# Performance work log

Hardware: AMD Instinct MI355X
Metric: run time of the kernel (lower is better)

Reference implementation:

```python
import jax, jax.numpy as jnp
import numpy as np
from jax import lax

B, N, C = 8, 16384, 4
NUM_GROUPS = 128
GROUP_SIZE = 32
GROUP_RADIUS = 0.1
UPSCALE_K = 128
OVERLAP_FACTOR = 0.7


def setup_inputs() -> dict:
    key = jax.random.key(0)
    k1, k2 = jax.random.split(key)
    # xyz in [0,1]^3, energy in [0,1] at channel 3
    points = jax.random.uniform(k1, (B, N, C), dtype=jnp.float32)
    lengths = jax.random.randint(k2, (B,), N // 2, N + 1).astype(jnp.int32)
    return {"points": points, "lengths": lengths}


def _fps(xyz, lengths, K):
    """Farthest point sampling. xyz: (B,N,3) -> centers (B,K,3), idx (B,K)."""
    B_, N_, _ = xyz.shape
    valid = jnp.arange(N_)[None, :] < lengths[:, None]          # (B,N)
    mind0 = jnp.where(valid, jnp.inf, -jnp.inf)                 # running min dist
    start = jnp.zeros((B_,), jnp.int32)                         # fixed start point
    batch = jnp.arange(B_)

    def step(carry, _):
        mind, cur = carry
        c = xyz[batch, cur]                                     # (B,3)
        d = jnp.sum((xyz - c[:, None, :]) ** 2, axis=-1)        # (B,N)
        mind = jnp.minimum(mind, jnp.where(valid, d, -jnp.inf))
        nxt = jnp.argmax(mind, axis=1).astype(jnp.int32)
        return (mind, nxt), cur

    _, idxs = lax.scan(step, (mind0, start), None, length=K)
    idxs = idxs.T                                               # (B,K)
    centers = xyz[batch[:, None], idxs]                         # (B,K,3)
    return centers, idxs


def _cnms(centers, radius, overlap_factor):
    """Greedy cluster-NMS over FPS-ordered centers. Returns keep mask (B,G)."""
    B_, G, _ = centers.shape
    d2 = jnp.sum((centers[:, :, None, :] - centers[:, None, :, :]) ** 2, axis=-1)
    thr = (2.0 * radius * (1.0 - overlap_factor)) ** 2          # spheres overlap > factor

    def step(keep, j):
        conflict = jnp.any(keep & (d2[:, j, :] < thr), axis=-1)
        keep = keep.at[:, j].set(~conflict)
        return keep, None

    keep, _ = lax.scan(step, jnp.zeros((B_, G), bool), jnp.arange(G))
    return keep


def _ball_query(centers, xyz, lengths, retain, K, radius):
    """First-K points within radius of each center (pytorch3d semantics); -1 pad."""
    N_ = xyz.shape[1]
    d2 = jnp.sum((centers[:, :, None, :] - xyz[:, None, :, :]) ** 2, axis=-1)  # (B,G,N)
    in_len = (jnp.arange(N_)[None, :] < lengths[:, None])[:, None, :]
    valid = (d2 <= radius * radius) & in_len & retain[:, :, None]
    # pick the K smallest point indices among valid ones -> "first K found"
    key_ = jnp.where(valid, jnp.arange(N_, dtype=jnp.int32)[None, None, :], N_)
    negv, _ = lax.top_k(-key_, K)                               # (B,G,K)
    idx = -negv
    return jnp.where(idx == N_, -1, idx)


def reference(points, lengths):
    xyz = points[..., :3]
    centers, _ = _fps(xyz, lengths, NUM_GROUPS)                 # (B,G,3)
    retain = _cnms(centers, GROUP_RADIUS, OVERLAP_FACTOR)       # (B,G)
    idx = _ball_query(centers, xyz, lengths, retain, UPSCALE_K, GROUP_RADIUS)

    # select_topk_by_energy (energies_idx = 3)
    batch = jnp.arange(points.shape[0])[:, None, None]
    invalid = idx == -1
    energies = jnp.where(invalid, -jnp.inf, points[batch, jnp.clip(idx, 0), 3])
    topv, topi = lax.top_k(energies, GROUP_SIZE)                # (B,G,K_new)
    tidx = jnp.take_along_axis(idx, topi, axis=2)
    tidx = jnp.where(jnp.isneginf(topv), -1, tidx)

    # fill_empty_indices: replace -1 with the group's first index
    fidx = jnp.where(tidx == -1, tidx[:, :, :1], tidx)

    # masked_gather: -1 -> gather 0 then zero out
    groups = points[batch, jnp.clip(fidx, 0)]                   # (B,G,K,C)
    groups = jnp.where((fidx == -1)[..., None], 0.0, groups)

    group_lengths = jnp.sum(jnp.all(tidx != -1, axis=2), axis=1)  # (B,)
    embedding_mask = jnp.arange(NUM_GROUPS)[None, :] < group_lengths[:, None]

    # center xyz channels, then scale ALL channels by radius (as in source)
    groups = groups.at[..., :3].add(-centers[:, :, None, :])
    groups = groups / GROUP_RADIUS
    return groups, centers, embedding_mask
```

## Files before the change

kernel.cpp:

```cpp
#include <hip/hip_runtime.h>
#include <math.h>

#define B_ 8
#define N_ 16384
#define G_ 128
#define GS_ 32
#define UK_ 128
#define FPS_T 1024
#define FPS_W 16
#define FPS_BLK 4
#define SLICE (N_ / FPS_BLK)
#define PPT (SLICE / FPS_T)
#define BQ_T 512
#define BQ_W 8

__device__ __forceinline__ float dist2(float x, float y, float z,
                                       float cx, float cy, float cz) {
    float dx = __fsub_rn(x, cx);
    float dy = __fsub_rn(y, cy);
    float dz = __fsub_rn(z, cz);
    return __fadd_rn(__fadd_rn(__fmul_rn(dx, dx), __fmul_rn(dy, dy)),
                     __fmul_rn(dz, dz));
}

__device__ __forceinline__ unsigned wave_umax_bcast(unsigned v) {
    unsigned t;
    t = (unsigned)__builtin_amdgcn_update_dpp(0, (int)v, 0x111, 0xf, 0xf, false); v = v > t ? v : t;
    t = (unsigned)__builtin_amdgcn_update_dpp(0, (int)v, 0x112, 0xf, 0xf, false); v = v > t ? v : t;
    t = (unsigned)__builtin_amdgcn_update_dpp(0, (int)v, 0x114, 0xf, 0xf, false); v = v > t ? v : t;
    t = (unsigned)__builtin_amdgcn_update_dpp(0, (int)v, 0x118, 0xf, 0xf, false); v = v > t ? v : t;
    t = (unsigned)__builtin_amdgcn_update_dpp(0, (int)v, 0x142, 0xa, 0xf, false); v = v > t ? v : t;
    t = (unsigned)__builtin_amdgcn_update_dpp(0, (int)v, 0x143, 0xc, 0xf, false); v = v > t ? v : t;
    return (unsigned)__builtin_amdgcn_readlane((int)v, 63);
}

__global__ __launch_bounds__(FPS_T, 4) void fps_cnms_kernel(
    const float4* __restrict__ pts, const int* __restrict__ lengths,
    float* __restrict__ centers_out, int* __restrict__ keep_out,
    unsigned long long* __restrict__ gslots, int* __restrict__ gl) {
    const int b = blockIdx.x & 7;
    const int slice = blockIdx.x >> 3;
    const int t = threadIdx.x;
    const int lane = t & 63;
    const int wv = t >> 6;
    const int len = lengths[b];
    const float4* p = pts + (size_t)b * N_;
    const int base = slice * SLICE;

    __shared__ float4 s_xy4[SLICE / 2];
    __shared__ unsigned long long s_part[2][FPS_W];
    __shared__ unsigned s_bc[2];
    __shared__ float s_cen[G_][3];

    if (slice == 0 && t == 0) gl[b] = 0;
    if (t < 2 * FPS_W) ((unsigned long long*)s_part)[t] = 0ull;
    if (t < 2) s_bc[t] = 0u;

    float zs[PPT], mind[PPT];
#pragma unroll
    for (int i2 = 0; i2 < PPT / 2; i2++) {
        int nA = base + (2 * i2) * FPS_T + t;
        int nB = base + (2 * i2 + 1) * FPS_T + t;
        float4 qA = p[nA];
        float4 qB = p[nB];
        s_xy4[i2 * FPS_T + t] = make_float4(qA.x, qA.y, qB.x, qB.y);
        zs[2 * i2]     = qA.z;
        zs[2 * i2 + 1] = qB.z;
        mind[2 * i2]     = (nA < len) ? INFINITY : -INFINITY;
        mind[2 * i2 + 1] = (nB < len) ? INFINITY : -INFINITY;
    }
    __syncthreads();

    int n = 0;
    for (int k = 0; k < G_; k++) {
        float4 c = p[n];
        float cx = c.x, cy = c.y, cz = c.z;
        if (slice == 0 && t == 0) {
            centers_out[(b * G_ + k) * 3 + 0] = cx;
            centers_out[(b * G_ + k) * 3 + 1] = cy;
            centers_out[(b * G_ + k) * 3 + 2] = cz;
            s_cen[k][0] = cx; s_cen[k][1] = cy; s_cen[k][2] = cz;
        }
        if (k == G_ - 1) break;

        float bv = -INFINITY;
        int bn = 0x7fffffff;
#pragma unroll
        for (int i2 = 0; i2 < PPT / 2; i2++) {
            float4 xy = s_xy4[i2 * FPS_T + t];
            float dA = dist2(xy.x, xy.y, zs[2 * i2],     cx, cy, cz);
            float dB = dist2(xy.z, xy.w, zs[2 * i2 + 1], cx, cy, cz);
            float mA = fminf(mind[2 * i2], dA);
            float mB = fminf(mind[2 * i2 + 1], dB);
            mind[2 * i2] = mA;
            mind[2 * i2 + 1] = mB;
            if (mA > bv) { bv = mA; bn = base + (2 * i2) * FPS_T + t; }
            if (mB > bv) { bv = mB; bn = base + (2 * i2 + 1) * FPS_T + t; }
        }
        unsigned u = __float_as_uint(bv);
        u = (u & 0x80000000u) ? ~u : (u | 0x80000000u);

        const unsigned stamp = (unsigned)(k + 1) << 14;

        unsigned wmax = wave_umax_bcast(u);
        unsigned ik = (u == wmax) ? ((unsigned)~bn & 0x3fffu) : 0u;
        unsigned wlo = wave_umax_bcast(ik);
        unsigned long long kk =
            ((unsigned long long)wmax << 32) | (stamp | wlo);

        if (lane == 0)
            __hip_atomic_store(&s_part[k & 1][wv], kk, __ATOMIC_RELAXED,
                               __HIP_MEMORY_SCOPE_WORKGROUP);

        unsigned nn;
        if (wv == 0) {
            unsigned long long v;
            do {
                v = __hip_atomic_load(&s_part[k & 1][lane & 15], __ATOMIC_RELAXED,
                                      __HIP_MEMORY_SCOPE_WORKGROUP);
            } while (__ballot(((unsigned)v >> 14) != (unsigned)(k + 1)) != 0ull);
            unsigned hi = (unsigned)(v >> 32);
            unsigned mh = wave_umax_bcast(hi);
            unsigned lo = (hi == mh) ? (unsigned)v : 0u;
            unsigned ml = wave_umax_bcast(lo);
            unsigned long long bkk = ((unsigned long long)mh << 32) | ml;

            unsigned long long* gs = gslots + (size_t)(k & 1) * 32 + b * FPS_BLK;
            if (lane == 0)
                __hip_atomic_store(&gs[slice], bkk, __ATOMIC_RELAXED,
                                   __HIP_MEMORY_SCOPE_AGENT);
            unsigned long long w;
            do {
                w = __hip_atomic_load(&gs[lane & 3], __ATOMIC_RELAXED,
                                      __HIP_MEMORY_SCOPE_AGENT);
            } while (__ballot(((unsigned)w >> 14) != (unsigned)(k + 1)) != 0ull);
            unsigned hi2 = (unsigned)(w >> 32);
            unsigned mh2 = wave_umax_bcast(hi2);
            unsigned lo2 = (hi2 == mh2) ? (unsigned)w : 0u;
            unsigned ml2 = wave_umax_bcast(lo2);
            nn = (unsigned)(~ml2) & 0x3fffu;
            if (lane == 0)
                __hip_atomic_store(&s_bc[k & 1], stamp | nn, __ATOMIC_RELAXED,
                                   __HIP_MEMORY_SCOPE_WORKGROUP);
        } else {
            unsigned s;
            do {
                s = __hip_atomic_load(&s_bc[k & 1], __ATOMIC_RELAXED,
                                      __HIP_MEMORY_SCOPE_WORKGROUP);
            } while ((s >> 14) != (unsigned)(k + 1));
            nn = s & 0x3fffu;
        }
        n = (int)nn;
    }

    if (slice == 0 && t < 64) {
        const float THR = (float)((2.0 * 0.1 * (1.0 - 0.7)) * (2.0 * 0.1 * (1.0 - 0.7)));
        float ax = s_cen[t][0],      ay = s_cen[t][1],      az = s_cen[t][2];
        float ex = s_cen[t + 64][0], ey = s_cen[t + 64][1], ez = s_cen[t + 64][2];
        bool k0 = false, k1 = false;
        for (int j = 0; j < G_; j++) {
            float jx = s_cen[j][0], jy = s_cen[j][1], jz = s_cen[j][2];
            bool c0 = k0 && (dist2(ax, ay, az, jx, jy, jz) < THR);
            bool c1 = k1 && (dist2(ex, ey, ez, jx, jy, jz) < THR);
            bool conflict = __any(c0 || c1);
            if (j == t)      k0 = !conflict;
            if (j == t + 64) k1 = !conflict;
        }
        keep_out[b * G_ + t]      = k0 ? 1 : 0;
        keep_out[b * G_ + t + 64] = k1 ? 1 : 0;
    }
}

__global__ __launch_bounds__(BQ_T) void group_kernel(
    const float4* __restrict__ pts, const int* __restrict__ lengths,
    const float* __restrict__ centers, const int* __restrict__ keep,
    float* __restrict__ groups_out, int* __restrict__ gl) {
    const int bid = blockIdx.x;
    const int b = bid >> 7;
    const int t = threadIdx.x;
    const int lane = t & 63;
    const int wv = t >> 6;

    const float cx = centers[bid * 3 + 0];
    const float cy = centers[bid * 3 + 1];
    const float cz = centers[bid * 3 + 2];
    float4* out4 = (float4*)(groups_out + (size_t)bid * GS_ * 4);

    if (!keep[bid]) {
        if (t < GS_) {
            float4 o;
            o.x = __fdiv_rn(__fsub_rn(0.f, cx), 0.1f);
            o.y = __fdiv_rn(__fsub_rn(0.f, cy), 0.1f);
            o.z = __fdiv_rn(__fsub_rn(0.f, cz), 0.1f);
            o.w = 0.f;
            out4[t] = o;
        }
        return;
    }

    __shared__ int   s_widx[BQ_W][UK_];
    __shared__ float s_wen[BQ_W][UK_];
    __shared__ int   s_wcnt[BQ_W];
    __shared__ int   s_list[UK_];
    __shared__ float s_en[UK_];
    __shared__ int   s_ord[GS_];

    const int len = lengths[b];
    const float R2 = (float)(0.1 * 0.1);
    const float4* p = pts + (size_t)b * N_;

    {
        const int base0 = wv * (N_ / BQ_W);
        int cnt = 0;
        for (int it = 0; it < (N_ / BQ_W) / 64; it++) {
            int n = base0 + it * 64 + lane;
            float4 q = p[n];
            float d2 = dist2(q.x, q.y, q.z, cx, cy, cz);
            bool pred = (n < len) && (d2 <= R2);
            unsigned long long m = __ballot(pred);
            int prefix = __popcll(m & ((1ull << lane) - 1ull));
            int slot = cnt + prefix;
            if (pred && slot < UK_) { s_widx[wv][slot] = n; s_wen[wv][slot] = q.w; }
            cnt += __popcll(m);
        }
        if (lane == 0) s_wcnt[wv] = (cnt < UK_) ? cnt : UK_;
    }
    __syncthreads();

    int M = 0;
#pragma unroll
    for (int w = 0; w < BQ_W; w++) M += s_wcnt[w];
    if (M > UK_) M = UK_;

    if (t < UK_ && t < M) {
        int j = t, w = 0;
        while (w < BQ_W - 1 && j >= s_wcnt[w]) { j -= s_wcnt[w]; w++; }
        s_list[t] = s_widx[w][j];
        s_en[t]   = s_wen[w][j];
    }
    __syncthreads();

    if (wv == 0) {
        float v0 = (lane < M) ? s_en[lane] : -INFINITY;
        float v1 = (lane + 64 < M) ? s_en[lane + 64] : -INFINITY;
        for (int k = 0; k < GS_; k++) {
            float bv; int bs;
            if (v0 >= v1) { bv = v0; bs = lane; }
            else          { bv = v1; bs = lane + 64; }
#pragma unroll
            for (int off = 32; off; off >>= 1) {
                float ov = __shfl_xor(bv, off);
                int   os = __shfl_xor(bs, off);
                bool tk = (ov > bv) || (ov == bv && os < bs);
                bv = tk ? ov : bv; bs = tk ? os : bs;
            }
            if (lane == 0) s_ord[k] = (bv == -INFINITY) ? -1 : bs;
            if (bs == lane)           v0 = -INFINITY;
            else if (bs == lane + 64) v1 = -INFINITY;
        }
    }
    __syncthreads();

    if (t < GS_) {
        int o0 = s_ord[0];
        int first = (o0 >= 0) ? s_list[o0] : -1;
        int ok = s_ord[t];
        int ti = (ok >= 0) ? s_list[ok] : -1;
        int f = (ti == -1) ? first : ti;
        float px = 0.f, py = 0.f, pz = 0.f, pw = 0.f;
        if (f >= 0) { float4 q = p[f]; px = q.x; py = q.y; pz = q.z; pw = q.w; }
        float4 o;
        o.x = __fdiv_rn(__fsub_rn(px, cx), 0.1f);
        o.y = __fdiv_rn(__fsub_rn(py, cy), 0.1f);
        o.z = __fdiv_rn(__fsub_rn(pz, cz), 0.1f);
        o.w = __fdiv_rn(pw, 0.1f);
        out4[t] = o;
    }
    if (t == 0 && M >= GS_) atomicAdd(&gl[b], 1);
}

__global__ void mask_kernel(const int* __restrict__ gl, float* __restrict__ mask_out) {
    int t = threadIdx.x;
    int b = t >> 7, g = t & 127;
    mask_out[t] = (g < gl[b]) ? 1.0f : 0.0f;
}

extern "C" void kernel_launch(void* const* d_in, const int* in_sizes, int n_in,
                              void* d_out, int out_size, void* d_ws, size_t ws_size,
                              hipStream_t stream) {
    const float4* pts = (const float4*)d_in[0];
    const int* lengths = (const int*)d_in[1];
    float* out = (float*)d_out;
    float* groups = out;
    float* centers = out + (size_t)B_ * G_ * GS_ * 4;
    float* mask = centers + (size_t)B_ * G_ * 3;
    unsigned long long* gslots = (unsigned long long*)d_ws;
    int* keep = (int*)(gslots + 64);
    int* gl = keep + B_ * G_;

    hipLaunchKernelGGL(fps_cnms_kernel, dim3(B_ * FPS_BLK), dim3(FPS_T), 0, stream,
                       pts, lengths, centers, keep, gslots, gl);
    hipLaunchKernelGGL(group_kernel, dim3(B_ * G_), dim3(BQ_T), 0, stream,
                       pts, lengths, centers, keep, groups, gl);
    hipLaunchKernelGGL(mask_kernel, dim3(1), dim3(B_ * G_), 0, stream, gl, mask);
}
```

Before: 306.7 us.

## Run FPS with one workgroup per batch, dropping cross-block global sync

Farthest point sampling moves from four cooperating workgroups per batch, which exchanged per-iteration argmax results through global atomics and spin-waits, to a single 1024-thread workgroup per batch that holds all 16384 points (16 per thread, xy in LDS). This removes the agent-scope global round trip on every one of the 127 iterations, but each thread now does four times more distance work and only 8 workgroups occupy the GPU. Waiting waves also add s_sleep in their LDS spin loop to reduce contention with the reducing wave.

```diff
diff --git a/kernel.cpp b/kernel.cpp
--- a/kernel.cpp
+++ b/kernel.cpp
@@ -8,9 +8,7 @@
 #define UK_ 128
 #define FPS_T 1024
 #define FPS_W 16
-#define FPS_BLK 4
-#define SLICE (N_ / FPS_BLK)
-#define PPT (SLICE / FPS_T)
+#define PPT (N_ / FPS_T)
 #define BQ_T 512
 #define BQ_W 8
 
@@ -37,30 +35,28 @@
 __global__ __launch_bounds__(FPS_T, 4) void fps_cnms_kernel(
     const float4* __restrict__ pts, const int* __restrict__ lengths,
     float* __restrict__ centers_out, int* __restrict__ keep_out,
-    unsigned long long* __restrict__ gslots, int* __restrict__ gl) {
-    const int b = blockIdx.x & 7;
-    const int slice = blockIdx.x >> 3;
+    int* __restrict__ gl) {
+    const int b = blockIdx.x;
     const int t = threadIdx.x;
     const int lane = t & 63;
     const int wv = t >> 6;
     const int len = lengths[b];
     const float4* p = pts + (size_t)b * N_;
-    const int base = slice * SLICE;
-
-    __shared__ float4 s_xy4[SLICE / 2];
+
+    __shared__ float4 s_xy4[N_ / 2];
     __shared__ unsigned long long s_part[2][FPS_W];
     __shared__ unsigned s_bc[2];
     __shared__ float s_cen[G_][3];
 
-    if (slice == 0 && t == 0) gl[b] = 0;
+    if (t == 0) gl[b] = 0;
     if (t < 2 * FPS_W) ((unsigned long long*)s_part)[t] = 0ull;
     if (t < 2) s_bc[t] = 0u;
 
     float zs[PPT], mind[PPT];
 #pragma unroll
     for (int i2 = 0; i2 < PPT / 2; i2++) {
-        int nA = base + (2 * i2) * FPS_T + t;
-        int nB = base + (2 * i2 + 1) * FPS_T + t;
+        int nA = (2 * i2) * FPS_T + t;
+        int nB = (2 * i2 + 1) * FPS_T + t;
         float4 qA = p[nA];
         float4 qB = p[nB];
         s_xy4[i2 * FPS_T + t] = make_float4(qA.x, qA.y, qB.x, qB.y);
@@ -75,7 +71,7 @@
     for (int k = 0; k < G_; k++) {
         float4 c = p[n];
         float cx = c.x, cy = c.y, cz = c.z;
-        if (slice == 0 && t == 0) {
+        if (t == 0) {
             centers_out[(b * G_ + k) * 3 + 0] = cx;
             centers_out[(b * G_ + k) * 3 + 1] = cy;
             centers_out[(b * G_ + k) * 3 + 2] = cz;
@@ -94,8 +90,8 @@
             float mB = fminf(mind[2 * i2 + 1], dB);
             mind[2 * i2] = mA;
             mind[2 * i2 + 1] = mB;
-            if (mA > bv) { bv = mA; bn = base + (2 * i2) * FPS_T + t; }
-            if (mB > bv) { bv = mB; bn = base + (2 * i2 + 1) * FPS_T + t; }
+            if (mA > bv) { bv = mA; bn = (2 * i2) * FPS_T + t; }
+            if (mB > bv) { bv = mB; bn = (2 * i2 + 1) * FPS_T + t; }
         }
         unsigned u = __float_as_uint(bv);
         u = (u & 0x80000000u) ? ~u : (u | 0x80000000u);
@@ -123,28 +119,14 @@
             unsigned mh = wave_umax_bcast(hi);
             unsigned lo = (hi == mh) ? (unsigned)v : 0u;
             unsigned ml = wave_umax_bcast(lo);
-            unsigned long long bkk = ((unsigned long long)mh << 32) | ml;
-
-            unsigned long long* gs = gslots + (size_t)(k & 1) * 32 + b * FPS_BLK;
-            if (lane == 0)
-                __hip_atomic_store(&gs[slice], bkk, __ATOMIC_RELAXED,
-                                   __HIP_MEMORY_SCOPE_AGENT);
-            unsigned long long w;
-            do {
-                w = __hip_atomic_load(&gs[lane & 3], __ATOMIC_RELAXED,
-                                      __HIP_MEMORY_SCOPE_AGENT);
-            } while (__ballot(((unsigned)w >> 14) != (unsigned)(k + 1)) != 0ull);
-            unsigned hi2 = (unsigned)(w >> 32);
-            unsigned mh2 = wave_umax_bcast(hi2);
-            unsigned lo2 = (hi2 == mh2) ? (unsigned)w : 0u;
-            unsigned ml2 = wave_umax_bcast(lo2);
-            nn = (unsigned)(~ml2) & 0x3fffu;
+            nn = (unsigned)(~ml) & 0x3fffu;
             if (lane == 0)
                 __hip_atomic_store(&s_bc[k & 1], stamp | nn, __ATOMIC_RELAXED,
                                    __HIP_MEMORY_SCOPE_WORKGROUP);
         } else {
             unsigned s;
             do {
+                __builtin_amdgcn_s_sleep(1);
                 s = __hip_atomic_load(&s_bc[k & 1], __ATOMIC_RELAXED,
                                       __HIP_MEMORY_SCOPE_WORKGROUP);
             } while ((s >> 14) != (unsigned)(k + 1));
@@ -153,7 +135,7 @@
         n = (int)nn;
     }
 
-    if (slice == 0 && t < 64) {
+    if (t < 64) {
         const float THR = (float)((2.0 * 0.1 * (1.0 - 0.7)) * (2.0 * 0.1 * (1.0 - 0.7)));
         float ax = s_cen[t][0],      ay = s_cen[t][1],      az = s_cen[t][2];
         float ex = s_cen[t + 64][0], ey = s_cen[t + 64][1], ez = s_cen[t + 64][2];
@@ -294,12 +276,11 @@
     float* groups = out;
     float* centers = out + (size_t)B_ * G_ * GS_ * 4;
     float* mask = centers + (size_t)B_ * G_ * 3;
-    unsigned long long* gslots = (unsigned long long*)d_ws;
-    int* keep = (int*)(gslots + 64);
+    int* keep = (int*)d_ws;
     int* gl = keep + B_ * G_;
 
-    hipLaunchKernelGGL(fps_cnms_kernel, dim3(B_ * FPS_BLK), dim3(FPS_T), 0, stream,
-                       pts, lengths, centers, keep, gslots, gl);
+    hipLaunchKernelGGL(fps_cnms_kernel, dim3(B_), dim3(FPS_T), 0, stream,
+                       pts, lengths, centers, keep, gl);
     hipLaunchKernelGGL(group_kernel, dim3(B_ * G_), dim3(BQ_T), 0, stream,
                        pts, lengths, centers, keep, groups, gl);
     hipLaunchKernelGGL(mask_kernel, dim3(1), dim3(B_ * G_), 0, stream, gl, mask);
```

Result: slower. 333.9 us (+8.9%).
